# Kernel tuning notes

Hardware: AMD Instinct MI355X
Metric: run time of the kernel (lower is better)

The kernel has to match this reference:

```python
import jax, jax.numpy as jnp
import numpy as np

B, T, A, K, STEPS, E = 2, 16384, 128, 128, 16, 126


def soft_dirac_last(x):
    # softmax forward-replaced by one-hot(argmax), straight-through backward
    sm = jax.nn.softmax(x, axis=-1)
    hard = jax.nn.one_hot(jnp.argmax(x, axis=-1), x.shape[-1], dtype=x.dtype)
    return sm + jax.lax.stop_gradient(hard - sm)


def _encode(x, d_unit, atom_embeddings):
    # x: (B,1,T); d_unit: (A,K) unit-norm atoms
    rng = jnp.linspace(0.0, 1.0, T, dtype=x.dtype)
    kernel = d_unit[:, None, :]  # OIH
    pad = [(K // 2, K - 1 - K // 2)]  # SAME
    batch_ix = jnp.arange(B)

    def step(res, _):
        # dense feature map: correlation of residual with every atom
        fm = jax.lax.conv_general_dilated(
            res, kernel, window_strides=(1,), padding=pad,
            dimension_numbers=("NCH", "OIH", "NCH"))  # (B,A,T)
        flat = fm.reshape(B, A * T)
        fi = jnp.argmax(flat, axis=-1)                      # sparsify n_to_keep=1
        value = jnp.take_along_axis(flat, fi[:, None], axis=-1)  # (B,1)
        ai = fi // T
        ti = fi % T
        # position: soft_dirac over time of sparse fm summed over atoms
        pos_row = jnp.zeros((B, T), x.dtype).at[batch_ix, ti].set(value[:, 0])
        pd = soft_dirac_last(pos_row)
        position = jnp.sum(pd * rng[None, :], axis=-1, keepdims=True) * 20.0  # (B,1)
        # atom one-hot: soft_dirac over atom axis of sparse fm summed over time
        atom_row = jnp.zeros((B, A), x.dtype).at[batch_ix, ai].set(value[:, 0])
        ad = soft_dirac_last(atom_row)
        ae = ad @ atom_embeddings  # (B,E)
        emb = jnp.concatenate([position, value, ae], axis=-1)  # (B, 2+E)
        # matching-pursuit residual update: subtract value * atom at found shift
        recon = value * d_unit[ai]  # (B,K)
        buf = jnp.zeros((B, T + K), x.dtype)
        buf = jax.vmap(lambda bb, rr, tt: jax.lax.dynamic_update_slice(bb, rr, (tt,)))(buf, recon, ti)
        res = res - buf[:, None, K // 2:K // 2 + T]
        return res, emb

    res, embs = jax.lax.scan(step, x, None, length=STEPS)
    embs = jnp.transpose(embs, (1, 0, 2))  # (B, STEPS, 2+E)
    return embs, res


def _canonical_ordering(embs, proj):
    keys = embs @ proj  # (B, STEPS)
    order = jnp.argsort(keys, axis=-1)
    return jnp.take_along_axis(embs, order[:, :, None], axis=1)


def setup_inputs() -> dict:
    key = jax.random.key(0)
    ks = jax.random.split(key, 5)
    return {
        "a": jax.random.normal(ks[0], (B, 1, T), jnp.float32),
        "b": jax.random.normal(ks[1], (B, 1, T), jnp.float32),
        "d": jax.random.normal(ks[2], (A, K), jnp.float32),
        "atom_embeddings": jax.random.normal(ks[3], (A, E), jnp.float32) * 0.1,
        "ordering_proj": jax.random.normal(ks[4], (128,), jnp.float32),
    }


def reference(a, b, d, atom_embeddings, ordering_proj):
    d_unit = d / (jnp.linalg.norm(d, axis=-1, keepdims=True) + 1e-8)
    ae, a_res = _encode(a, d_unit, atom_embeddings)
    be, b_res = _encode(b, d_unit, atom_embeddings)
    ae = _canonical_ordering(ae, ordering_proj)
    be = _canonical_ordering(be, ordering_proj)
    a_norm = jnp.linalg.norm(a_res.reshape(-1, T), axis=-1)
    b_norm = jnp.linalg.norm(b_res.reshape(-1, T), axis=-1)
    return jnp.mean((ae - be) ** 2) + jnp.mean(jnp.abs(a_norm - b_norm))
```

## Files before the change

kernel.cpp:

```cpp
#include <hip/hip_runtime.h>
#include <math.h>

#define T_DIM 16384
#define A_DIM 128
#define K_DIM 128
#define N_STEPS 16
#define E_DIM 126
#define NSEQ 4

#define ATI 8
#define NAT 16
#define TT 256
#define NTT 64
#define NPT 1024
#define NCB 64
#define HB 8192
#define RL_LEN 8319
#define RL_PAD 8608
#define SS_LEN 383
#define SS_PAD 404

#define PIDX(i) ((i) + ((i) >> 5))

__device__ inline unsigned long long pack_vi(float v, int fi) {
    unsigned int b = __float_as_uint(v);
    b = (b & 0x80000000u) ? ~b : (b | 0x80000000u);
    return ((unsigned long long)b << 32) | (unsigned int)(~fi);
}
__device__ inline void unpack_vi(unsigned long long p, float* v, int* fi) {
    unsigned int lo = (unsigned int)(p & 0xffffffffu);
    unsigned int b = (unsigned int)(p >> 32);
    unsigned int fb = (b & 0x80000000u) ? (b & 0x7fffffffu) : ~b;
    *v = __uint_as_float(fb);
    *fi = (int)(~lo);
}
__device__ inline unsigned long long u64max(unsigned long long a, unsigned long long b) {
    return a > b ? a : b;
}

__global__ __launch_bounds__(256) void k_prep(
    const float* __restrict__ d, float* __restrict__ du,
    unsigned long long* __restrict__ zeroU, int* __restrict__ cnt,
    float* __restrict__ norm2) {
    int blk = blockIdx.x, tid = threadIdx.x;
    if (blk < 128) {
        __shared__ float s[128];
        float v = 0.0f;
        if (tid < 128) { v = d[blk * K_DIM + tid]; s[tid] = v * v; }
        __syncthreads();
        for (int off = 64; off > 0; off >>= 1) {
            if (tid < off) s[tid] += s[tid + off];
            __syncthreads();
        }
        if (tid < 128) du[blk * K_DIM + tid] = v / (sqrtf(s[0]) + 1e-8f);
    } else {
        for (int i = tid; i < 1984; i += 256) zeroU[i] = 0ULL;
        if (tid < NSEQ) { cnt[tid] = 0; norm2[tid] = 0.0f; }
    }
}

__device__ inline unsigned long long tile_compute(
    const float* __restrict__ duP, const float* __restrict__ rsh,
    int L0, int a_lo, int t_lo, int tid, unsigned long long* red4) {

    float acc[2][4];
    #pragma unroll
    for (int i = 0; i < 2; i++)
        #pragma unroll
        for (int j = 0; j < 4; j++) acc[i][j] = 0.0f;

    float r[8];
    #pragma unroll
    for (int m = 0; m < 8; m++) r[m] = rsh[PIDX(L0 + m)];

    #pragma unroll 4
    for (int k = 0; k < K_DIM; k += 4) {
        float dA[2][4];
        #pragma unroll
        for (int i = 0; i < 2; i++)
            *(float4*)dA[i] = *(const float4*)(duP + i * K_DIM + k);
        #pragma unroll
        for (int dk = 0; dk < 4; dk++) {
            #pragma unroll
            for (int i = 0; i < 2; i++) {
                float s = dA[i][dk];
                #pragma unroll
                for (int j = 0; j < 4; j++)
                    acc[i][j] = fmaf(s, r[j + dk], acc[i][j]);
            }
        }
        r[0] = r[4]; r[1] = r[5]; r[2] = r[6]; r[3] = r[7];
        #pragma unroll
        for (int m = 0; m < 4; m++) r[4 + m] = rsh[PIDX(L0 + k + 8 + m)];
    }

    float bv = -INFINITY;
    int bi = 0x7fffffff;
    #pragma unroll
    for (int i = 0; i < 2; i++) {
        int a = a_lo + i;
        #pragma unroll
        for (int j = 0; j < 4; j++) {
            int fi = a * T_DIM + t_lo + j;
            float v = acc[i][j];
            if (v > bv || (v == bv && fi < bi)) { bv = v; bi = fi; }
        }
    }
    #pragma unroll
    for (int off = 32; off > 0; off >>= 1) {
        float v2 = __shfl_down(bv, off);
        int   i2 = __shfl_down(bi, off);
        if (v2 > bv || (v2 == bv && i2 < bi)) { bv = v2; bi = i2; }
    }
    if ((tid & 63) == 0) red4[tid >> 6] = pack_vi(bv, bi);
    __syncthreads();
    if (tid == 0) {
        unsigned long long m = red4[0];
        #pragma unroll
        for (int w = 1; w < 4; w++) m = u64max(m, red4[w]);
        red4[0] = m;
    }
    __syncthreads();
    return red4[0];
}

__global__ __launch_bounds__(256) void k_step_full(
    const float* __restrict__ a, const float* __restrict__ b,
    const float* __restrict__ du, const float* __restrict__ ae,
    float* __restrict__ emb, unsigned long long* __restrict__ pmax,
    int* __restrict__ cnt, int* __restrict__ dirty0,
    unsigned long long* __restrict__ w0slot) {

    int seq = blockIdx.y;
    int blk = blockIdx.x;
    int a_base = (blk >> 6) * ATI;
    int t0 = (blk & 63) * TT;
    int tid = threadIdx.x;

    __shared__ float rsh[SS_PAD];
    __shared__ unsigned long long red4[4];
    __shared__ unsigned long long pm_sh[256];
    __shared__ int last_flag;

    const float* x = (seq < 2 ? a : b) + (seq & 1) * T_DIM;
    for (int i = tid; i < SS_LEN; i += 256) {
        int t = t0 - 64 + i;
        rsh[PIDX(i)] = (t >= 0 && t < T_DIM) ? x[t] : 0.0f;
    }
    __syncthreads();

    int tg = tid & 63;
    int ag = __builtin_amdgcn_readfirstlane(tid >> 6);
    unsigned long long p = tile_compute(du + (a_base + ag * 2) * K_DIM, rsh,
                                        4 * tg, a_base + ag * 2, t0 + 4 * tg,
                                        tid, red4);
    if (tid == 0) {
        pmax[seq * NPT + blk] = p;
        __threadfence();
        last_flag = (atomicAdd(&cnt[seq], 1) == NPT - 1);
    }
    __syncthreads();
    if (!last_flag) return;

    __threadfence();
    {
        unsigned long long m = u64max(pmax[seq * NPT + tid],
                                      pmax[seq * NPT + 256 + tid]);
        m = u64max(m, u64max(pmax[seq * NPT + 512 + tid],
                             pmax[seq * NPT + 768 + tid]));
        pm_sh[tid] = m;
    }
    __syncthreads();
    for (int off = 128; off > 0; off >>= 1) {
        if (tid < off) pm_sh[tid] = u64max(pm_sh[tid], pm_sh[tid + off]);
        __syncthreads();
    }
    float value; int fi;
    unpack_vi(pm_sh[0], &value, &fi);
    int ai = fi >> 14;
    int ti = fi & (T_DIM - 1);
    int pos_idx = value > 0.0f ? ti : 0;
    int atom_idx = value > 0.0f ? ai : 0;

    float* e = emb + (seq * N_STEPS + 0) * 128;
    if (tid == 0) {
        e[0] = ((float)pos_idx / (float)(T_DIM - 1)) * 20.0f;
        e[1] = value;
        int nlo = ti - (K_DIM - 1); if (nlo < 0) nlo = 0;
        int nhi = ti + K_DIM;       if (nhi > T_DIM) nhi = T_DIM;
        dirty0[seq * 2 + 0] = nlo;
        dirty0[seq * 2 + 1] = nhi;
        w0slot[seq] = pm_sh[0];
    }
    if (tid >= 2 && tid < 2 + E_DIM) e[tid] = ae[atom_idx * E_DIM + tid - 2];
}

__global__ __launch_bounds__(256) void k_inc(
    const float* __restrict__ a, const float* __restrict__ b,
    const float* __restrict__ du, const float* __restrict__ ae,
    float* __restrict__ emb, const unsigned long long* __restrict__ pmax,
    unsigned long long* __restrict__ dslots,
    unsigned long long* __restrict__ wslot,
    const unsigned long long* __restrict__ w0slot,
    const int* __restrict__ dirty0, float* __restrict__ norm2) {

    int seq = blockIdx.y;
    int blk = blockIdx.x;
    int tid = threadIdx.x;

    if (blk == NCB) {
        __shared__ unsigned long long table[NPT];
        __shared__ unsigned long long red4[4];
        for (int i = tid; i < NPT; i += 256) table[i] = pmax[seq * NPT + i];
        int lo = dirty0[seq * 2 + 0];
        int hi = dirty0[seq * 2 + 1];
        __syncthreads();

        for (int step = 1; step < N_STEPS; step++) {
            int T0 = lo >> 8, T1 = T0 + 1;
            bool hasT1 = (T1 < NTT) && (T1 * TT < hi);
            if (tid < 2 * NAT) {
                int at = tid >> 1, w = tid & 1;
                if (w == 0 || hasT1) {
                    const unsigned long long* sp =
                        &dslots[((step - 1) * NSEQ + seq) * (2 * NAT) + tid];
                    unsigned long long v = __hip_atomic_load(sp, __ATOMIC_RELAXED,
                                                             __HIP_MEMORY_SCOPE_AGENT);
                    while (v == 0ULL) {
                        __builtin_amdgcn_s_sleep(1);
                        v = __hip_atomic_load(sp, __ATOMIC_RELAXED,
                                              __HIP_MEMORY_SCOPE_AGENT);
                    }
                    table[at * NTT + (w ? T1 : T0)] = v;
                }
            }
            __syncthreads();
            unsigned long long m = u64max(table[tid], table[tid + 256]);
            m = u64max(m, u64max(table[tid + 512], table[tid + 768]));
            #pragma unroll
            for (int off = 32; off > 0; off >>= 1)
                m = u64max(m, __shfl_down(m, off));
            if ((tid & 63) == 0) red4[tid >> 6] = m;
            __syncthreads();
            unsigned long long w;
            if (tid == 0) {
                w = red4[0];
                #pragma unroll
                for (int j = 1; j < 4; j++) w = u64max(w, red4[j]);
                red4[0] = w;
                atomicExch(&wslot[(step - 1) * NSEQ + seq], w);
            }
            __syncthreads();
            w = red4[0];
            float value; int fi;
            unpack_vi(w, &value, &fi);
            int ti = fi & (T_DIM - 1);
            int ai = fi >> 14;
            int pos_idx = value > 0.0f ? ti : 0;
            int atom_idx = value > 0.0f ? ai : 0;
            float* e = emb + (seq * N_STEPS + step) * 128;
            if (tid == 0) {
                e[0] = ((float)pos_idx / (float)(T_DIM - 1)) * 20.0f;
                e[1] = value;
            }
            if (tid >= 2 && tid < 128) e[tid] = ae[atom_idx * E_DIM + tid - 2];
            lo = ti - (K_DIM - 1); if (lo < 0) lo = 0;
            hi = ti + K_DIM;       if (hi > T_DIM) hi = T_DIM;
        }
        return;
    }

    int atile = blk >> 2;
    int half = (blk >> 1) & 1;
    int par = blk & 1;
    int a_base = atile * ATI;
    int base = half * HB;

    __shared__ float resL[RL_PAD];
    __shared__ unsigned long long red4[4];
    __shared__ unsigned long long wsh;
    __shared__ float w0v_s; __shared__ int w0t_s, w0a_s;
    __shared__ float snorm[256];

    if (tid == 0) {
        float v; int fi;
        unpack_vi(w0slot[seq], &v, &fi);
        w0v_s = v; w0t_s = fi & (T_DIM - 1); w0a_s = fi >> 14;
    }
    __syncthreads();
    float w0v = w0v_s; int w0t = w0t_s, w0a = w0a_s;

    const float* x = (seq < 2 ? a : b) + (seq & 1) * T_DIM;
    for (int i = tid; i < RL_LEN; i += 256) {
        int t = base - 64 + i;
        float v = 0.0f;
        if (t >= 0 && t < T_DIM) {
            v = x[t];
            int dk = t - (w0t - K_DIM / 2);
            if (dk >= 0 && dk < K_DIM)
                v = __fsub_rn(v, __fmul_rn(w0v, du[w0a * K_DIM + dk]));
        }
        resL[PIDX(i)] = v;
    }
    int lo = dirty0[seq * 2 + 0];
    int hi = dirty0[seq * 2 + 1];
    __syncthreads();

    for (int step = 1; step < N_STEPS; step++) {
        int T0 = lo >> 8, T1 = T0 + 1;
        int cand = -1;
        if (((T0 & 1) == par) && ((T0 >> 5) == half)) cand = T0;
        else if (T1 < NTT && ((T1 & 1) == par) && ((T1 >> 5) == half) &&
                 T1 * TT < hi) cand = T1;

        if (cand >= 0) {
            int t0 = cand * TT;
            int tg = tid & 63;
            int ag = __builtin_amdgcn_readfirstlane(tid >> 6);
            unsigned long long p = tile_compute(
                du + (a_base + ag * 2) * K_DIM, resL,
                (t0 - base) + 4 * tg, a_base + ag * 2, t0 + 4 * tg, tid, red4);
            if (tid == 0)
                atomicExch(&dslots[((step - 1) * NSEQ + seq) * (2 * NAT) +
                                   atile * 2 + (cand == T1 ? 1 : 0)], p);
        }
        if (tid == 0) {
            const unsigned long long* sp = &wslot[(step - 1) * NSEQ + seq];
            unsigned long long v = __hip_atomic_load(sp, __ATOMIC_RELAXED,
                                                     __HIP_MEMORY_SCOPE_AGENT);
            while (v == 0ULL) {
                __builtin_amdgcn_s_sleep(2);
                v = __hip_atomic_load(sp, __ATOMIC_RELAXED,
                                      __HIP_MEMORY_SCOPE_AGENT);
            }
            wsh = v;
        }
        __syncthreads();

        float value; int fi;
        unpack_vi(wsh, &value, &fi);
        int ti = fi & (T_DIM - 1);
        int ai = fi >> 14;
        if (tid < 128) {
            int t = ti - K_DIM / 2 + tid;
            if (t >= 0 && t < T_DIM) {
                int L = t - base + 64;
                if (L >= 0 && L < RL_LEN) {
                    float r = resL[PIDX(L)];
                    resL[PIDX(L)] = __fsub_rn(r, __fmul_rn(value, du[ai * K_DIM + tid]));
                }
            }
        }
        __syncthreads();
        lo = ti - (K_DIM - 1); if (lo < 0) lo = 0;
        hi = ti + K_DIM;       if (hi > T_DIM) hi = T_DIM;
    }

    if (atile == 0 && par == 0) {
        float s = 0.0f;
        for (int t = tid; t < HB; t += 256) {
            float v = resL[PIDX(t + 64)];
            s = fmaf(v, v, s);
        }
        snorm[tid] = s;
        __syncthreads();
        for (int off = 128; off > 0; off >>= 1) {
            if (tid < off) snorm[tid] += snorm[tid + off];
            __syncthreads();
        }
        if (tid == 0) atomicAdd(&norm2[seq], snorm[0]);
    }
}

__global__ __launch_bounds__(1024) void k_tail(
    const float* __restrict__ emb, const float* __restrict__ proj,
    const float* __restrict__ norm2, float* __restrict__ out) {
    int tid = threadIdx.x;
    __shared__ float sh[1024];
    __shared__ float norms[NSEQ];
    __shared__ float keys[NSEQ][N_STEPS];
    __shared__ int   order[NSEQ][N_STEPS];

    if (tid < NSEQ) norms[tid] = sqrtf(norm2[tid]);
    {
        int pair = tid >> 4;
        int seq = pair >> 4, st = pair & 15;
        int ln = tid & 15;
        const float* e = emb + (seq * N_STEPS + st) * 128 + ln * 8;
        const float* pr = proj + ln * 8;
        float kk = 0.0f;
        #pragma unroll
        for (int dd = 0; dd < 8; dd++) kk = fmaf(e[dd], pr[dd], kk);
        sh[tid] = kk;
        __syncthreads();
        for (int off = 8; off > 0; off >>= 1) {
            if (ln < off) sh[tid] += sh[tid + off];
            __syncthreads();
        }
        if (ln == 0) keys[seq][st] = sh[tid];
        __syncthreads();
    }
    if (tid < NSEQ) {
        int ord[N_STEPS];
        for (int i = 0; i < N_STEPS; i++) ord[i] = i;
        for (int i = 1; i < N_STEPS; i++) {
            int oi = ord[i];
            float kv = keys[tid][oi];
            int j = i - 1;
            while (j >= 0 && keys[tid][ord[j]] > kv) { ord[j + 1] = ord[j]; j--; }
            ord[j + 1] = oi;
        }
        for (int i = 0; i < N_STEPS; i++) order[tid][i] = ord[i];
    }
    __syncthreads();
    float s = 0.0f;
    #pragma unroll
    for (int t = 0; t < 4; t++) {
        int idx = tid + t * 1024;
        int bq = idx >> 11;
        int st = (idx >> 7) & 15;
        int dd = idx & 127;
        float va = emb[((bq    ) * N_STEPS + order[bq    ][st]) * 128 + dd];
        float vb = emb[((2 + bq) * N_STEPS + order[2 + bq][st]) * 128 + dd];
        float df = va - vb;
        s = fmaf(df, df, s);
    }
    sh[tid] = s;
    __syncthreads();
    for (int off = 512; off > 0; off >>= 1) {
        if (tid < off) sh[tid] += sh[tid + off];
        __syncthreads();
    }
    if (tid == 0) {
        float mse = sh[0] / 4096.0f;
        float mad = 0.5f * (fabsf(norms[0] - norms[2]) + fabsf(norms[1] - norms[3]));
        out[0] = mse + mad;
    }
}

extern "C" void kernel_launch(void* const* d_in, const int* in_sizes, int n_in,
                              void* d_out, int out_size, void* d_ws, size_t ws_size,
                              hipStream_t stream) {
    const float* a    = (const float*)d_in[0];
    const float* b    = (const float*)d_in[1];
    const float* d    = (const float*)d_in[2];
    const float* ae   = (const float*)d_in[3];
    const float* proj = (const float*)d_in[4];
    float* out = (float*)d_out;

    float* ws  = (float*)d_ws;
    float* du  = ws;
    float* emb = du + A_DIM * K_DIM;
    unsigned long long* pmax   = (unsigned long long*)(emb + NSEQ * N_STEPS * 128);
    unsigned long long* dslots = pmax + NSEQ * NPT;
    unsigned long long* wslot  = dslots + (N_STEPS - 1) * NSEQ * 2 * NAT;
    unsigned long long* w0slot = wslot + (N_STEPS - 1) * NSEQ;
    int* cnt    = (int*)(w0slot + NSEQ);
    int* dirty0 = cnt + NSEQ;
    float* norm2 = (float*)(dirty0 + 2 * NSEQ);

    k_prep<<<129, 256, 0, stream>>>(d, du, dslots, cnt, norm2);

    dim3 gfull(NPT, NSEQ);
    k_step_full<<<gfull, 256, 0, stream>>>(a, b, du, ae, emb, pmax, cnt,
                                           dirty0, w0slot);

    dim3 ginc(NCB + 1, NSEQ);
    k_inc<<<ginc, 256, 0, stream>>>(a, b, du, ae, emb, pmax, dslots, wslot,
                                    w0slot, dirty0, norm2);

    k_tail<<<1, 1024, 0, stream>>>(emb, proj, norm2, out);
}
```

Baseline: 248.2 us.

## Merge step0, incremental steps and tail into one persistent mega-kernel

```diff
diff --git a/kernel.cpp b/kernel.cpp
--- a/kernel.cpp
+++ b/kernel.cpp
@@ -8,19 +8,22 @@
 #define E_DIM 126
 #define NSEQ 4
 
-#define ATI 8
-#define NAT 16
+#define NPT0 512
+#define NAT8 16
 #define TT 256
 #define NTT 64
-#define NPT 1024
-#define NCB 64
 #define HB 8192
 #define RL_LEN 8319
-#define RL_PAD 8608
 #define SS_LEN 383
-#define SS_PAD 404
+#define SPAD 16
 
 #define PIDX(i) ((i) + ((i) >> 5))
+
+#define NB_STEP0 (NPT0 * NSEQ)
+#define NB_INC   (65 * NSEQ)
+#define NB_TOTAL (NB_STEP0 + NB_INC + 1)
+
+#define SM_U64 4448
 
 __device__ inline unsigned long long pack_vi(float v, int fi) {
     unsigned int b = __float_as_uint(v);
@@ -37,11 +40,19 @@
 __device__ inline unsigned long long u64max(unsigned long long a, unsigned long long b) {
     return a > b ? a : b;
 }
+__device__ inline unsigned long long pollu64(const unsigned long long* p) {
+    unsigned long long v = __hip_atomic_load(p, __ATOMIC_RELAXED,
+                                             __HIP_MEMORY_SCOPE_AGENT);
+    while (v == 0ULL) {
+        __builtin_amdgcn_s_sleep(1);
+        v = __hip_atomic_load(p, __ATOMIC_RELAXED, __HIP_MEMORY_SCOPE_AGENT);
+    }
+    return v;
+}
 
 __global__ __launch_bounds__(256) void k_prep(
     const float* __restrict__ d, float* __restrict__ du,
-    unsigned long long* __restrict__ zeroU, int* __restrict__ cnt,
-    float* __restrict__ norm2) {
+    unsigned long long* __restrict__ arena) {
     int blk = blockIdx.x, tid = threadIdx.x;
     if (blk < 128) {
         __shared__ float s[128];
@@ -54,25 +65,92 @@
         }
         if (tid < 128) du[blk * K_DIM + tid] = v / (sqrtf(s[0]) + 1e-8f);
     } else {
-        for (int i = tid; i < 1984; i += 256) zeroU[i] = 0ULL;
-        if (tid < NSEQ) { cnt[tid] = 0; norm2[tid] = 0.0f; }
-    }
-}
-
-__device__ inline unsigned long long tile_compute(
+        int zb = blk - 128;
+        for (int i = zb * 256 + tid; i < 31744; i += 64 * 256)
+            arena[2048 + i] = 0ULL;
+        if (blk == 128) {
+            int* ctrl = (int*)(arena + 33792);
+            if (tid < NSEQ) {
+                ctrl[tid * 32] = 0;
+                ((float*)ctrl)[160 + tid * 32] = 0.0f;
+            }
+            if (tid == 4) ctrl[128] = 0;
+        }
+    }
+}
+
+__device__ inline unsigned long long tile16(
     const float* __restrict__ duP, const float* __restrict__ rsh,
     int L0, int a_lo, int t_lo, int tid, unsigned long long* red4) {
-
+    float acc[4][4];
+    #pragma unroll
+    for (int i = 0; i < 4; i++)
+        #pragma unroll
+        for (int j = 0; j < 4; j++) acc[i][j] = 0.0f;
+    float r[8];
+    #pragma unroll
+    for (int m = 0; m < 8; m++) r[m] = rsh[PIDX(L0 + m)];
+    #pragma unroll 4
+    for (int k = 0; k < K_DIM; k += 4) {
+        float dA[4][4];
+        #pragma unroll
+        for (int i = 0; i < 4; i++)
+            *(float4*)dA[i] = *(const float4*)(duP + i * K_DIM + k);
+        #pragma unroll
+        for (int dk = 0; dk < 4; dk++) {
+            #pragma unroll
+            for (int i = 0; i < 4; i++) {
+                float s = dA[i][dk];
+                #pragma unroll
+                for (int j = 0; j < 4; j++)
+                    acc[i][j] = fmaf(s, r[j + dk], acc[i][j]);
+            }
+        }
+        r[0] = r[4]; r[1] = r[5]; r[2] = r[6]; r[3] = r[7];
+        #pragma unroll
+        for (int m = 0; m < 4; m++) r[4 + m] = rsh[PIDX(L0 + k + 8 + m)];
+    }
+    float bv = -INFINITY;
+    int bi = 0x7fffffff;
+    #pragma unroll
+    for (int i = 0; i < 4; i++) {
+        int aa = a_lo + i;
+        #pragma unroll
+        for (int j = 0; j < 4; j++) {
+            int fi = aa * T_DIM + t_lo + j;
+            float v = acc[i][j];
+            if (v > bv || (v == bv && fi < bi)) { bv = v; bi = fi; }
+        }
+    }
+    #pragma unroll
+    for (int off = 32; off > 0; off >>= 1) {
+        float v2 = __shfl_down(bv, off);
+        int   i2 = __shfl_down(bi, off);
+        if (v2 > bv || (v2 == bv && i2 < bi)) { bv = v2; bi = i2; }
+    }
+    if ((tid & 63) == 0) red4[tid >> 6] = pack_vi(bv, bi);
+    __syncthreads();
+    if (tid == 0) {
+        unsigned long long m = red4[0];
+        #pragma unroll
+        for (int w = 1; w < 4; w++) m = u64max(m, red4[w]);
+        red4[0] = m;
+    }
+    __syncthreads();
+    return red4[0];
+}
+
+__device__ inline unsigned long long tile8(
+    const float* __restrict__ duP, const float* __restrict__ rsh,
+    int L0, int a_lo, int t_lo, int tid, unsigned long long* red4) {
     float acc[2][4];
     #pragma unroll
     for (int i = 0; i < 2; i++)
         #pragma unroll
         for (int j = 0; j < 4; j++) acc[i][j] = 0.0f;
-
     float r[8];
     #pragma unroll
     for (int m = 0; m < 8; m++) r[m] = rsh[PIDX(L0 + m)];
-
     #pragma unroll 4
     for (int k = 0; k < K_DIM; k += 4) {
         float dA[2][4];
@@ -93,15 +171,14 @@
         #pragma unroll
         for (int m = 0; m < 4; m++) r[4 + m] = rsh[PIDX(L0 + k + 8 + m)];
     }
-
     float bv = -INFINITY;
     int bi = 0x7fffffff;
     #pragma unroll
     for (int i = 0; i < 2; i++) {
-        int a = a_lo + i;
+        int aa = a_lo + i;
         #pragma unroll
         for (int j = 0; j < 4; j++) {
-            int fi = a * T_DIM + t_lo + j;
+            int fi = aa * T_DIM + t_lo + j;
             float v = acc[i][j];
             if (v > bv || (v == bv && fi < bi)) { bv = v; bi = fi; }
         }
@@ -124,317 +201,309 @@
     return red4[0];
 }
 
-__global__ __launch_bounds__(256) void k_step_full(
+__global__ __launch_bounds__(256) void k_mega(
     const float* __restrict__ a, const float* __restrict__ b,
     const float* __restrict__ du, const float* __restrict__ ae,
-    float* __restrict__ emb, unsigned long long* __restrict__ pmax,
-    int* __restrict__ cnt, int* __restrict__ dirty0,
-    unsigned long long* __restrict__ w0slot) {
-
-    int seq = blockIdx.y;
-    int blk = blockIdx.x;
-    int a_base = (blk >> 6) * ATI;
-    int t0 = (blk & 63) * TT;
-    int tid = threadIdx.x;
-
-    __shared__ float rsh[SS_PAD];
-    __shared__ unsigned long long red4[4];
-    __shared__ unsigned long long pm_sh[256];
-    __shared__ int last_flag;
-
-    const float* x = (seq < 2 ? a : b) + (seq & 1) * T_DIM;
-    for (int i = tid; i < SS_LEN; i += 256) {
-        int t = t0 - 64 + i;
-        rsh[PIDX(i)] = (t >= 0 && t < T_DIM) ? x[t] : 0.0f;
-    }
-    __syncthreads();
-
-    int tg = tid & 63;
-    int ag = __builtin_amdgcn_readfirstlane(tid >> 6);
-    unsigned long long p = tile_compute(du + (a_base + ag * 2) * K_DIM, rsh,
-                                        4 * tg, a_base + ag * 2, t0 + 4 * tg,
-                                        tid, red4);
-    if (tid == 0) {
-        pmax[seq * NPT + blk] = p;
-        __threadfence();
-        last_flag = (atomicAdd(&cnt[seq], 1) == NPT - 1);
-    }
-    __syncthreads();
-    if (!last_flag) return;
-
-    __threadfence();
-    {
-        unsigned long long m = u64max(pmax[seq * NPT + tid],
-                                      pmax[seq * NPT + 256 + tid]);
-        m = u64max(m, u64max(pmax[seq * NPT + 512 + tid],
-                             pmax[seq * NPT + 768 + tid]));
-        pm_sh[tid] = m;
-    }
-    __syncthreads();
-    for (int off = 128; off > 0; off >>= 1) {
-        if (tid < off) pm_sh[tid] = u64max(pm_sh[tid], pm_sh[tid + off]);
-        __syncthreads();
-    }
-    float value; int fi;
-    unpack_vi(pm_sh[0], &value, &fi);
-    int ai = fi >> 14;
-    int ti = fi & (T_DIM - 1);
-    int pos_idx = value > 0.0f ? ti : 0;
-    int atom_idx = value > 0.0f ? ai : 0;
-
-    float* e = emb + (seq * N_STEPS + 0) * 128;
-    if (tid == 0) {
-        e[0] = ((float)pos_idx / (float)(T_DIM - 1)) * 20.0f;
-        e[1] = value;
-        int nlo = ti - (K_DIM - 1); if (nlo < 0) nlo = 0;
-        int nhi = ti + K_DIM;       if (nhi > T_DIM) nhi = T_DIM;
-        dirty0[seq * 2 + 0] = nlo;
-        dirty0[seq * 2 + 1] = nhi;
-        w0slot[seq] = pm_sh[0];
-    }
-    if (tid >= 2 && tid < 2 + E_DIM) e[tid] = ae[atom_idx * E_DIM + tid - 2];
-}
-
-__global__ __launch_bounds__(256) void k_inc(
-    const float* __restrict__ a, const float* __restrict__ b,
-    const float* __restrict__ du, const float* __restrict__ ae,
-    float* __restrict__ emb, const unsigned long long* __restrict__ pmax,
-    unsigned long long* __restrict__ dslots,
-    unsigned long long* __restrict__ wslot,
-    const unsigned long long* __restrict__ w0slot,
-    const int* __restrict__ dirty0, float* __restrict__ norm2) {
-
-    int seq = blockIdx.y;
+    const float* __restrict__ proj, float* __restrict__ emb,
+    unsigned long long* __restrict__ arena, float* __restrict__ out) {
+
+    __shared__ unsigned long long SMEM[SM_U64];
+    unsigned long long* pmax = arena;
+    unsigned long long* dsl  = arena + 2048;
+    unsigned long long* wsl  = arena + 32768;
+    unsigned long long* w0   = arena + 33728;
+    int*   cnt   = (int*)(arena + 33792);
+    int*   done  = cnt + 128;
+    float* norm2 = (float*)cnt + 160;
+
     int blk = blockIdx.x;
     int tid = threadIdx.x;
 
-    if (blk == NCB) {
-        __shared__ unsigned long long table[NPT];
-        __shared__ unsigned long long red4[4];
-        for (int i = tid; i < NPT; i += 256) table[i] = pmax[seq * NPT + i];
-        int lo = dirty0[seq * 2 + 0];
-        int hi = dirty0[seq * 2 + 1];
-        __syncthreads();
-
-        for (int step = 1; step < N_STEPS; step++) {
-            int T0 = lo >> 8, T1 = T0 + 1;
-            bool hasT1 = (T1 < NTT) && (T1 * TT < hi);
-            if (tid < 2 * NAT) {
-                int at = tid >> 1, w = tid & 1;
-                if (w == 0 || hasT1) {
-                    const unsigned long long* sp =
-                        &dslots[((step - 1) * NSEQ + seq) * (2 * NAT) + tid];
-                    unsigned long long v = __hip_atomic_load(sp, __ATOMIC_RELAXED,
-                                                             __HIP_MEMORY_SCOPE_AGENT);
-                    while (v == 0ULL) {
-                        __builtin_amdgcn_s_sleep(1);
-                        v = __hip_atomic_load(sp, __ATOMIC_RELAXED,
-                                              __HIP_MEMORY_SCOPE_AGENT);
-                    }
-                    table[at * NTT + (w ? T1 : T0)] = v;
-                }
-            }
-            __syncthreads();
-            unsigned long long m = u64max(table[tid], table[tid + 256]);
-            m = u64max(m, u64max(table[tid + 512], table[tid + 768]));
-            #pragma unroll
-            for (int off = 32; off > 0; off >>= 1)
-                m = u64max(m, __shfl_down(m, off));
-            if ((tid & 63) == 0) red4[tid >> 6] = m;
-            __syncthreads();
-            unsigned long long w;
-            if (tid == 0) {
-                w = red4[0];
+    if (blk < NB_STEP0) {
+        int seq = blk >> 9;
+        int idx = blk & 511;
+        int a_base = (idx >> 6) * 16;
+        int t0 = (idx & 63) * TT;
+        float* rsh = (float*)SMEM;
+        unsigned long long* pm_sh = SMEM + 256;
+        unsigned long long* red4  = SMEM + 512;
+        int* flag = (int*)(SMEM + 516);
+
+        const float* x = (seq < 2 ? a : b) + (seq & 1) * T_DIM;
+        for (int i = tid; i < SS_LEN; i += 256) {
+            int t = t0 - 64 + i;
+            rsh[PIDX(i)] = (t >= 0 && t < T_DIM) ? x[t] : 0.0f;
+        }
+        __syncthreads();
+        int tg = tid & 63;
+        int ag = __builtin_amdgcn_readfirstlane(tid >> 6);
+        unsigned long long p = tile16(du + (a_base + ag * 4) * K_DIM, rsh,
+                                      4 * tg, a_base + ag * 4, t0 + 4 * tg,
+                                      tid, red4);
+        if (tid == 0) {
+            pmax[seq * NPT0 + idx] = p;
+            __threadfence();
+            flag[0] = (atomicAdd(&cnt[seq * 32], 1) == NPT0 - 1);
+        }
+        __syncthreads();
+        if (!flag[0]) return;
+
+        __threadfence();
+        pm_sh[tid] = u64max(pmax[seq * NPT0 + tid], pmax[seq * NPT0 + 256 + tid]);
+        __syncthreads();
+        for (int off = 128; off > 0; off >>= 1) {
+            if (tid < off) pm_sh[tid] = u64max(pm_sh[tid], pm_sh[tid + off]);
+            __syncthreads();
+        }
+        float value; int fi;
+        unpack_vi(pm_sh[0], &value, &fi);
+        int ai = fi >> 14, ti = fi & (T_DIM - 1);
+        int pos_idx = value > 0.0f ? ti : 0;
+        int atom_idx = value > 0.0f ? ai : 0;
+        float* e = emb + (seq * N_STEPS + 0) * 128;
+        if (tid == 0) {
+            e[0] = ((float)pos_idx / (float)(T_DIM - 1)) * 20.0f;
+            e[1] = value;
+        }
+        if (tid >= 2 && tid < 2 + E_DIM) e[tid] = ae[atom_idx * E_DIM + tid - 2];
+        __syncthreads();
+        __threadfence();
+        if (tid == 0) atomicExch(&w0[seq * SPAD], pm_sh[0]);
+        return;
+    }
+
+    if (blk < NB_STEP0 + NB_INC) {
+        int r = blk - NB_STEP0;
+        int seq = r / 65;
+        int sub = r - seq * 65;
+
+        if (sub == 64) {
+            unsigned long long* table   = SMEM;
+            unsigned long long* poll_sh = SMEM + 512;
+            unsigned long long* red4    = SMEM + 548;
+            unsigned long long* wbc     = SMEM + 552;
+
+            if (tid == 0) wbc[0] = pollu64(&w0[seq * SPAD]);
+            __syncthreads();
+            __threadfence();
+            for (int i = tid; i < NPT0; i += 256) table[i] = pmax[seq * NPT0 + i];
+            float v0; int fi0;
+            unpack_vi(wbc[0], &v0, &fi0);
+            int ti = fi0 & (T_DIM - 1);
+            int lo = ti - 127; if (lo < 0) lo = 0;
+            int hi = ti + 128; if (hi > T_DIM) hi = T_DIM;
+            __syncthreads();
+
+            for (int step = 1; step < N_STEPS; step++) {
+                int T0 = lo >> 8, T1 = T0 + 1;
+                bool hasT1 = (T1 < NTT) && (T1 * TT < hi);
+                if (tid < 32) {
+                    if (((tid & 1) == 0) || hasT1)
+                        poll_sh[tid] = pollu64(
+                            &dsl[(((step - 1) * NSEQ + seq) * 32 + tid) * SPAD]);
+                }
+                __syncthreads();
+                if (tid < 16) {
+                    int at16 = tid >> 1, ts = tid & 1;
+                    if (ts == 0 || hasT1)
+                        table[at16 * 64 + (ts ? T1 : T0)] =
+                            u64max(poll_sh[at16 * 4 + ts], poll_sh[at16 * 4 + 2 + ts]);
+                }
+                __syncthreads();
+                unsigned long long m = u64max(table[tid], table[tid + 256]);
                 #pragma unroll
-                for (int j = 1; j < 4; j++) w = u64max(w, red4[j]);
-                red4[0] = w;
-                atomicExch(&wslot[(step - 1) * NSEQ + seq], w);
-            }
-            __syncthreads();
-            w = red4[0];
-            float value; int fi;
-            unpack_vi(w, &value, &fi);
-            int ti = fi & (T_DIM - 1);
-            int ai = fi >> 14;
-            int pos_idx = value > 0.0f ? ti : 0;
-            int atom_idx = value > 0.0f ? ai : 0;
-            float* e = emb + (seq * N_STEPS + step) * 128;
-            if (tid == 0) {
-                e[0] = ((float)pos_idx / (float)(T_DIM - 1)) * 20.0f;
-                e[1] = value;
-            }
-            if (tid >= 2 && tid < 128) e[tid] = ae[atom_idx * E_DIM + tid - 2];
-            lo = ti - (K_DIM - 1); if (lo < 0) lo = 0;
-            hi = ti + K_DIM;       if (hi > T_DIM) hi = T_DIM;
-        }
-        return;
-    }
-
-    int atile = blk >> 2;
-    int half = (blk >> 1) & 1;
-    int par = blk & 1;
-    int a_base = atile * ATI;
-    int base = half * HB;
-
-    __shared__ float resL[RL_PAD];
-    __shared__ unsigned long long red4[4];
-    __shared__ unsigned long long wsh;
-    __shared__ float w0v_s; __shared__ int w0t_s, w0a_s;
-    __shared__ float snorm[256];
-
-    if (tid == 0) {
-        float v; int fi;
-        unpack_vi(w0slot[seq], &v, &fi);
-        w0v_s = v; w0t_s = fi & (T_DIM - 1); w0a_s = fi >> 14;
-    }
-    __syncthreads();
-    float w0v = w0v_s; int w0t = w0t_s, w0a = w0a_s;
-
-    const float* x = (seq < 2 ? a : b) + (seq & 1) * T_DIM;
-    for (int i = tid; i < RL_LEN; i += 256) {
-        int t = base - 64 + i;
-        float v = 0.0f;
-        if (t >= 0 && t < T_DIM) {
-            v = x[t];
-            int dk = t - (w0t - K_DIM / 2);
-            if (dk >= 0 && dk < K_DIM)
-                v = __fsub_rn(v, __fmul_rn(w0v, du[w0a * K_DIM + dk]));
-        }
-        resL[PIDX(i)] = v;
-    }
-    int lo = dirty0[seq * 2 + 0];
-    int hi = dirty0[seq * 2 + 1];
-    __syncthreads();
-
-    for (int step = 1; step < N_STEPS; step++) {
-        int T0 = lo >> 8, T1 = T0 + 1;
-        int cand = -1;
-        if (((T0 & 1) == par) && ((T0 >> 5) == half)) cand = T0;
-        else if (T1 < NTT && ((T1 & 1) == par) && ((T1 >> 5) == half) &&
-                 T1 * TT < hi) cand = T1;
-
-        if (cand >= 0) {
-            int t0 = cand * TT;
-            int tg = tid & 63;
-            int ag = __builtin_amdgcn_readfirstlane(tid >> 6);
-            unsigned long long p = tile_compute(
-                du + (a_base + ag * 2) * K_DIM, resL,
-                (t0 - base) + 4 * tg, a_base + ag * 2, t0 + 4 * tg, tid, red4);
-            if (tid == 0)
-                atomicExch(&dslots[((step - 1) * NSEQ + seq) * (2 * NAT) +
-                                   atile * 2 + (cand == T1 ? 1 : 0)], p);
-        }
-        if (tid == 0) {
-            const unsigned long long* sp = &wslot[(step - 1) * NSEQ + seq];
-            unsigned long long v = __hip_atomic_load(sp, __ATOMIC_RELAXED,
-                                                     __HIP_MEMORY_SCOPE_AGENT);
-            while (v == 0ULL) {
-                __builtin_amdgcn_s_sleep(2);
-                v = __hip_atomic_load(sp, __ATOMIC_RELAXED,
-                                      __HIP_MEMORY_SCOPE_AGENT);
-            }
-            wsh = v;
-        }
-        __syncthreads();
-
-        float value; int fi;
-        unpack_vi(wsh, &value, &fi);
-        int ti = fi & (T_DIM - 1);
-        int ai = fi >> 14;
+                for (int off = 32; off > 0; off >>= 1)
+                    m = u64max(m, __shfl_down(m, off));
+                if ((tid & 63) == 0) red4[tid >> 6] = m;
+                __syncthreads();
+                if (tid == 0) {
+                    unsigned long long w = red4[0];
+                    #pragma unroll
+                    for (int j = 1; j < 4; j++) w = u64max(w, red4[j]);
+                    red4[0] = w;
+                    atomicExch(&wsl[((step - 1) * NSEQ + seq) * SPAD], w);
+                }
+                __syncthreads();
+                float value; int fi;
+                unpack_vi(red4[0], &value, &fi);
+                int wt = fi & (T_DIM - 1);
+                int wa = fi >> 14;
+                int pos_idx = value > 0.0f ? wt : 0;
+                int atom_idx = value > 0.0f ? wa : 0;
+                float* e = emb + (seq * N_STEPS + step) * 128;
+                if (tid == 0) {
+                    e[0] = ((float)pos_idx / (float)(T_DIM - 1)) * 20.0f;
+                    e[1] = value;
+                }
+                if (tid >= 2 && tid < 128) e[tid] = ae[atom_idx * E_DIM + tid - 2];
+                lo = wt - 127; if (lo < 0) lo = 0;
+                hi = wt + 128; if (hi > T_DIM) hi = T_DIM;
+            }
+            __syncthreads();
+            __threadfence();
+            if (tid == 0) atomicAdd(done, 1);
+            return;
+        }
+
+        int atile = sub >> 2;
+        int half = (sub >> 1) & 1;
+        int par = sub & 1;
+        int a_base = atile * 8;
+        int base = half * HB;
+        float* resL = (float*)SMEM;
+        unsigned long long* red4 = SMEM + 4304;
+        unsigned long long* wshp = SMEM + 4308;
+        float* snorm = (float*)(SMEM + 4320);
+
+        const float* x = (seq < 2 ? a : b) + (seq & 1) * T_DIM;
+        for (int i = tid; i < RL_LEN; i += 256) {
+            int t = base - 64 + i;
+            resL[PIDX(i)] = (t >= 0 && t < T_DIM) ? x[t] : 0.0f;
+        }
+        if (tid == 0) wshp[0] = pollu64(&w0[seq * SPAD]);
+        __syncthreads();
+        float v0; int fi0;
+        unpack_vi(wshp[0], &v0, &fi0);
+        int ti0 = fi0 & (T_DIM - 1), ai0 = fi0 >> 14;
         if (tid < 128) {
-            int t = ti - K_DIM / 2 + tid;
+            int t = ti0 - 64 + tid;
             if (t >= 0 && t < T_DIM) {
                 int L = t - base + 64;
                 if (L >= 0 && L < RL_LEN) {
-                    float r = resL[PIDX(L)];
-                    resL[PIDX(L)] = __fsub_rn(r, __fmul_rn(value, du[ai * K_DIM + tid]));
-                }
-            }
-        }
-        __syncthreads();
-        lo = ti - (K_DIM - 1); if (lo < 0) lo = 0;
-        hi = ti + K_DIM;       if (hi > T_DIM) hi = T_DIM;
-    }
-
-    if (atile == 0 && par == 0) {
+                    float rr = resL[PIDX(L)];
+                    resL[PIDX(L)] = __fsub_rn(rr, __fmul_rn(v0, du[ai0 * K_DIM + tid]));
+                }
+            }
+        }
+        __syncthreads();
+        int lo = ti0 - 127; if (lo < 0) lo = 0;
+        int hi = ti0 + 128; if (hi > T_DIM) hi = T_DIM;
+
+        for (int step = 1; step < N_STEPS; step++) {
+            int T0 = lo >> 8, T1 = T0 + 1;
+            int cand = -1;
+            if (((T0 & 1) == par) && ((T0 >> 5) == half)) cand = T0;
+            else if (T1 < NTT && ((T1 & 1) == par) && ((T1 >> 5) == half) &&
+                     T1 * TT < hi) cand = T1;
+
+            if (cand >= 0) {
+                int t0 = cand * TT;
+                int tg = tid & 63;
+                int ag = __builtin_amdgcn_readfirstlane(tid >> 6);
+                unsigned long long p = tile8(
+                    du + (a_base + ag * 2) * K_DIM, resL,
+                    (t0 - base) + 4 * tg, a_base + ag * 2, t0 + 4 * tg, tid, red4);
+                if (tid == 0)
+                    atomicExch(&dsl[(((step - 1) * NSEQ + seq) * 32 +
+                                     atile * 2 + (cand == T1 ? 1 : 0)) * SPAD], p);
+            }
+            if (tid == 0) wshp[0] = pollu64(&wsl[((step - 1) * NSEQ + seq) * SPAD]);
+            __syncthreads();
+            float value; int fi;
+            unpack_vi(wshp[0], &value, &fi);
+            int wt = fi & (T_DIM - 1);
+            int wa = fi >> 14;
+            if (tid < 128) {
+                int t = wt - 64 + tid;
+                if (t >= 0 && t < T_DIM) {
+                    int L = t - base + 64;
+                    if (L >= 0 && L < RL_LEN) {
+                        float rr = resL[PIDX(L)];
+                        resL[PIDX(L)] = __fsub_rn(rr, __fmul_rn(value, du[wa * K_DIM + tid]));
+                    }
+                }
+            }
+            __syncthreads();
+            lo = wt - 127; if (lo < 0) lo = 0;
+            hi = wt + 128; if (hi > T_DIM) hi = T_DIM;
+        }
+
+        if (atile == 0 && par == 0) {
+            float s = 0.0f;
+            for (int t = tid; t < HB; t += 256) {
+                float v = resL[PIDX(t + 64)];
+                s = fmaf(v, v, s);
+            }
+            snorm[tid] = s;
+            __syncthreads();
+            for (int off = 128; off > 0; off >>= 1) {
+                if (tid < off) snorm[tid] += snorm[tid + off];
+                __syncthreads();
+            }
+            if (tid == 0) {
+                float old = atomicAdd(&norm2[seq * 32], snorm[0]);
+                if (__float_as_uint(old) != 0xFFFFFFFFu)
+                    atomicAdd(done, 1);
+            }
+        }
+        return;
+    }
+
+    {
+        float* keys  = (float*)SMEM;
+        int*   order = (int*)(SMEM + 32);
+        float* sh    = (float*)(SMEM + 64);
+        float* norms = (float*)(SMEM + 192);
+
+        if (tid == 0) {
+            int c = __hip_atomic_load(done, __ATOMIC_RELAXED, __HIP_MEMORY_SCOPE_AGENT);
+            while (c < 12) {
+                __builtin_amdgcn_s_sleep(8);
+                c = __hip_atomic_load(done, __ATOMIC_RELAXED, __HIP_MEMORY_SCOPE_AGENT);
+            }
+        }
+        __syncthreads();
+        __threadfence();
+
+        if (tid < NSEQ)
+            norms[tid] = sqrtf(__hip_atomic_load(&norm2[tid * 32], __ATOMIC_RELAXED,
+                                                 __HIP_MEMORY_SCOPE_AGENT));
+        if (tid < 64) {
+            int seq = tid >> 4, st = tid & 15;
+            const float* e = emb + (seq * N_STEPS + st) * 128;
+            float kk = 0.0f;
+            for (int dd = 0; dd < 128; dd++) kk = fmaf(e[dd], proj[dd], kk);
+            keys[tid] = kk;
+        }
+        __syncthreads();
+        if (tid < NSEQ) {
+            int ord[N_STEPS];
+            for (int i = 0; i < N_STEPS; i++) ord[i] = i;
+            for (int i = 1; i < N_STEPS; i++) {
+                int oi = ord[i];
+                float kv = keys[tid * N_STEPS + oi];
+                int j = i - 1;
+                while (j >= 0 && keys[tid * N_STEPS + ord[j]] > kv) {
+                    ord[j + 1] = ord[j]; j--;
+                }
+                ord[j + 1] = oi;
+            }
+            for (int i = 0; i < N_STEPS; i++) order[tid * N_STEPS + i] = ord[i];
+        }
+        __syncthreads();
         float s = 0.0f;
-        for (int t = tid; t < HB; t += 256) {
-            float v = resL[PIDX(t + 64)];
-            s = fmaf(v, v, s);
-        }
-        snorm[tid] = s;
+        #pragma unroll
+        for (int t = 0; t < 16; t++) {
+            int idx = tid + t * 256;
+            int bq = idx >> 11;
+            int st = (idx >> 7) & 15;
+            int dd = idx & 127;
+            float va = emb[((bq    ) * N_STEPS + order[bq * N_STEPS + st]) * 128 + dd];
+            float vb = emb[((2 + bq) * N_STEPS + order[(2 + bq) * N_STEPS + st]) * 128 + dd];
+            float df = va - vb;
+            s = fmaf(df, df, s);
+        }
+        sh[tid] = s;
         __syncthreads();
         for (int off = 128; off > 0; off >>= 1) {
-            if (tid < off) snorm[tid] += snorm[tid + off];
-            __syncthreads();
-        }
-        if (tid == 0) atomicAdd(&norm2[seq], snorm[0]);
-    }
-}
-
-__global__ __launch_bounds__(1024) void k_tail(
-    const float* __restrict__ emb, const float* __restrict__ proj,
-    const float* __restrict__ norm2, float* __restrict__ out) {
-    int tid = threadIdx.x;
-    __shared__ float sh[1024];
-    __shared__ float norms[NSEQ];
-    __shared__ float keys[NSEQ][N_STEPS];
-    __shared__ int   order[NSEQ][N_STEPS];
-
-    if (tid < NSEQ) norms[tid] = sqrtf(norm2[tid]);
-    {
-        int pair = tid >> 4;
-        int seq = pair >> 4, st = pair & 15;
-        int ln = tid & 15;
-        const float* e = emb + (seq * N_STEPS + st) * 128 + ln * 8;
-        const float* pr = proj + ln * 8;
-        float kk = 0.0f;
-        #pragma unroll
-        for (int dd = 0; dd < 8; dd++) kk = fmaf(e[dd], pr[dd], kk);
-        sh[tid] = kk;
-        __syncthreads();
-        for (int off = 8; off > 0; off >>= 1) {
-            if (ln < off) sh[tid] += sh[tid + off];
-            __syncthreads();
-        }
-        if (ln == 0) keys[seq][st] = sh[tid];
-        __syncthreads();
-    }
-    if (tid < NSEQ) {
-        int ord[N_STEPS];
-        for (int i = 0; i < N_STEPS; i++) ord[i] = i;
-        for (int i = 1; i < N_STEPS; i++) {
-            int oi = ord[i];
-            float kv = keys[tid][oi];
-            int j = i - 1;
-            while (j >= 0 && keys[tid][ord[j]] > kv) { ord[j + 1] = ord[j]; j--; }
-            ord[j + 1] = oi;
-        }
-        for (int i = 0; i < N_STEPS; i++) order[tid][i] = ord[i];
-    }
-    __syncthreads();
-    float s = 0.0f;
-    #pragma unroll
-    for (int t = 0; t < 4; t++) {
-        int idx = tid + t * 1024;
-        int bq = idx >> 11;
-        int st = (idx >> 7) & 15;
-        int dd = idx & 127;
-        float va = emb[((bq    ) * N_STEPS + order[bq    ][st]) * 128 + dd];
-        float vb = emb[((2 + bq) * N_STEPS + order[2 + bq][st]) * 128 + dd];
-        float df = va - vb;
-        s = fmaf(df, df, s);
-    }
-    sh[tid] = s;
-    __syncthreads();
-    for (int off = 512; off > 0; off >>= 1) {
-        if (tid < off) sh[tid] += sh[tid + off];
-        __syncthreads();
-    }
-    if (tid == 0) {
-        float mse = sh[0] / 4096.0f;
-        float mad = 0.5f * (fabsf(norms[0] - norms[2]) + fabsf(norms[1] - norms[3]));
-        out[0] = mse + mad;
+            if (tid < off) sh[tid] += sh[tid + off];
+            __syncthreads();
+        }
+        if (tid == 0) {
+            float mse = sh[0] / 4096.0f;
+            float mad = 0.5f * (fabsf(norms[0] - norms[2]) + fabsf(norms[1] - norms[3]));
+            out[0] = mse + mad;
+        }
     }
 }
 
@@ -451,23 +520,8 @@
     float* ws  = (float*)d_ws;
     float* du  = ws;
     float* emb = du + A_DIM * K_DIM;
-    unsigned long long* pmax   = (unsigned long long*)(emb + NSEQ * N_STEPS * 128);
-    unsigned long long* dslots = pmax + NSEQ * NPT;
-    unsigned long long* wslot  = dslots + (N_STEPS - 1) * NSEQ * 2 * NAT;
-    unsigned long long* w0slot = wslot + (N_STEPS - 1) * NSEQ;
-    int* cnt    = (int*)(w0slot + NSEQ);
-    int* dirty0 = cnt + NSEQ;
-    float* norm2 = (float*)(dirty0 + 2 * NSEQ);
-
-    k_prep<<<129, 256, 0, stream>>>(d, du, dslots, cnt, norm2);
-
-    dim3 gfull(NPT, NSEQ);
-    k_step_full<<<gfull, 256, 0, stream>>>(a, b, du, ae, emb, pmax, cnt,
-                                           dirty0, w0slot);
-
-    dim3 ginc(NCB + 1, NSEQ);
-    k_inc<<<ginc, 256, 0, stream>>>(a, b, du, ae, emb, pmax, dslots, wslot,
-                                    w0slot, dirty0, norm2);
-
-    k_tail<<<1, 1024, 0, stream>>>(emb, proj, norm2, out);
-}
+    unsigned long long* arena = (unsigned long long*)(emb + NSEQ * N_STEPS * 128);
+
+    k_prep<<<192, 256, 0, stream>>>(d, du, arena);
+    k_mega<<<NB_TOTAL, 256, 0, stream>>>(a, b, du, ae, proj, emb, arena, out);
+}
```

New measurement: 214.5 us. 13.5% less time.
